# Performance work log

Measured on AMD Instinct MI355X. Metric: run time of the kernel, lower is better.

The kernel has to match this reference:

```python
import jax, jax.numpy as jnp
import numpy as np

NUM_CLUSTERS = 64
MARGIN = 1.0
B = 8192


def setup_inputs() -> dict:
    key = jax.random.key(0)
    k1, k2, k3 = jax.random.split(key, 3)
    features = jax.random.normal(k1, (B, 128), dtype=jnp.float32)
    cluster_labels = jax.random.randint(k2, (B,), 0, NUM_CLUSTERS)
    manifold_coords = jax.random.normal(k3, (B, 2), dtype=jnp.float32)
    return {"features": features, "cluster_labels": cluster_labels,
            "manifold_coords": manifold_coords}


def _pairwise_dist(x):
    # Euclidean cdist via the (|a|^2 + |b|^2 - 2ab) identity; [B, B]
    sq = jnp.sum(x * x, axis=1)
    d2 = sq[:, None] + sq[None, :] - 2.0 * (x @ x.T)
    d2 = jnp.maximum(d2, 0.0)
    # Overwrite diagonal (same-point zero distance) to avoid sqrt(0); diagonal
    # entries only feed the discarded intra-cluster M[i,i] values.
    idx = jnp.arange(x.shape[0])
    d2 = jnp.where(idx[:, None] == idx[None, :], 1.0, d2)
    return jnp.sqrt(d2)


def reference(features, cluster_labels, manifold_coords):
    # Equivalent to the torch double loop over unique labels: min pairwise
    # distance between every cluster pair (i < j), hinge with margin, mean.
    d = _pairwise_dist(manifold_coords)                       # [B, B]
    # segment-min over rows then columns -> min distance per cluster pair
    row_min = jax.ops.segment_min(d, cluster_labels, num_segments=NUM_CLUSTERS)      # [K, B]
    M = jax.ops.segment_min(row_min.T, cluster_labels, num_segments=NUM_CLUSTERS).T  # [K, K]
    upper = jnp.triu(jnp.ones((NUM_CLUSTERS, NUM_CLUSTERS), dtype=bool), k=1)
    hinge = jax.nn.relu(MARGIN - M)
    num_pairs = NUM_CLUSTERS * (NUM_CLUSTERS - 1) // 2
    return jnp.sum(jnp.where(upper, hinge, 0.0)) / num_pairs
```

## Files before the change

### kernel.cpp

```cpp
#include <hip/hip_runtime.h>

#define B_N 8192
#define K_CL 64
#define CAP 256
#define INF_F 3.0e38f


__global__ __launch_bounds__(256) void gather_kernel(
    const int* __restrict__ labels, const float2* __restrict__ coords,
    float2* __restrict__ lists, int* __restrict__ cnts) {
    int c = blockIdx.x;
    __shared__ int cnt;
    int tid = threadIdx.x;
    int lane = tid & 63;
    if (tid == 0) cnt = 0;
    __syncthreads();
#pragma unroll
    for (int k = 0; k < 8; ++k) {
        int v4 = tid + k * 256;
        int4 lb = reinterpret_cast<const int4*>(labels)[v4];
        int lab[4] = {lb.x, lb.y, lb.z, lb.w};
#pragma unroll
        for (int cc = 0; cc < 4; ++cc) {
            bool m = (lab[cc] == c);
            unsigned long long mask = __ballot(m);
            if (mask) {
                int wb = 0;
                if (lane == 0) wb = atomicAdd(&cnt, __popcll(mask));
                wb = __shfl(wb, 0, 64);
                if (m) {
                    int pos = wb + __popcll(mask & ((1ull << lane) - 1));
                    if (pos < CAP) lists[c * CAP + pos] = coords[v4 * 4 + cc];
                }
            }
        }
    }
    __syncthreads();
    if (tid == 0) cnts[c] = min(cnt, CAP);
}

__global__ __launch_bounds__(256) void pair_min_kernel(
    const float2* __restrict__ lists, const int* __restrict__ cnts,
    float* __restrict__ hinges) {
    int ci = blockIdx.x, cj = blockIdx.y;
    if (ci >= cj) return;
    int nI = cnts[ci], nJ = cnts[cj];
    int tid = threadIdx.x;
    __shared__ float2 jpt[CAP];
    if (tid < nJ) jpt[tid] = lists[cj * CAP + tid];
    bool valid = tid < nI;
    float2 pi = make_float2(0.0f, 0.0f);
    if (valid) pi = lists[ci * CAP + tid];
    __syncthreads();

    float m0 = INF_F, m1 = INF_F, m2 = INF_F, m3 = INF_F;
    if (valid) {
        int j = 0;
        for (; j + 3 < nJ; j += 4) {
            float2 a = jpt[j], b = jpt[j + 1], c = jpt[j + 2], d = jpt[j + 3];
            float dx0 = pi.x - a.x, dy0 = pi.y - a.y;
            float dx1 = pi.x - b.x, dy1 = pi.y - b.y;
            float dx2 = pi.x - c.x, dy2 = pi.y - c.y;
            float dx3 = pi.x - d.x, dy3 = pi.y - d.y;
            m0 = fminf(m0, dx0 * dx0 + dy0 * dy0);
            m1 = fminf(m1, dx1 * dx1 + dy1 * dy1);
            m2 = fminf(m2, dx2 * dx2 + dy2 * dy2);
            m3 = fminf(m3, dx3 * dx3 + dy3 * dy3);
        }
        for (; j < nJ; ++j) {
            float dx = pi.x - jpt[j].x, dy = pi.y - jpt[j].y;
            m0 = fminf(m0, dx * dx + dy * dy);
        }
    }
    float myMin = fminf(fminf(m0, m1), fminf(m2, m3));

    for (int off = 32; off > 0; off >>= 1)
        myMin = fminf(myMin, __shfl_down(myMin, off, 64));
    __shared__ float wmin[4];
    int wave = tid >> 6, lane = tid & 63;
    if (lane == 0) wmin[wave] = myMin;
    __syncthreads();
    if (tid == 0) {
        float m = fminf(fminf(wmin[0], wmin[1]), fminf(wmin[2], wmin[3]));
        float h = 1.0f - sqrtf(m);
        hinges[ci * K_CL + cj] = h > 0.0f ? h : 0.0f;
    }
}

__global__ void reduce_hinge_kernel(const float* __restrict__ hinges,
                                    float* __restrict__ out) {
    int tid = threadIdx.x;
    float s = 0.0f;
    for (int p = tid; p < K_CL * K_CL; p += 256) {
        int ci = p >> 6, cj = p & 63;
        if (ci < cj) s += hinges[p];
    }
    for (int off = 32; off > 0; off >>= 1)
        s += __shfl_down(s, off, 64);
    __shared__ float wsum[4];
    int wave = tid >> 6, lane = tid & 63;
    if (lane == 0) wsum[wave] = s;
    __syncthreads();
    if (tid == 0)
        out[0] = (wsum[0] + wsum[1] + wsum[2] + wsum[3]) / 2016.0f;
}

extern "C" void kernel_launch(void* const* d_in, const int* in_sizes, int n_in,
                              void* d_out, int out_size, void* d_ws, size_t ws_size,
                              hipStream_t stream) {
    const int*    labels = (const int*)d_in[1];
    const float2* coords = (const float2*)d_in[2];
    float* out = (float*)d_out;

    float2* lists  = (float2*)d_ws;
    int*    cnts   = (int*)((float*)d_ws + 2 * K_CL * CAP);
    float*  hinges = (float*)d_ws + 2 * K_CL * CAP + 64;

    gather_kernel<<<K_CL, 256, 0, stream>>>(labels, coords, lists, cnts);
    dim3 grid(K_CL, K_CL);
    pair_min_kernel<<<grid, 256, 0, stream>>>(lists, cnts, hinges);
    reduce_hinge_kernel<<<1, 256, 0, stream>>>(hinges, out);
}
```

Measured before the change: 29.70 us.

## Fuse hinge reduction into pair kernel via last-block atomic counter

Launches only the 2016 upper-triangle cluster pairs as a 1D grid instead of a 64x64 grid where half the blocks exit early. The final hinge sum moves into the pair kernel: each block increments an atomic counter, and the last block to finish sums all hinges. This removes one kernel launch and the empty blocks. In exchange it adds a memset launch to reset the counter, a serial loop in each block to decode the pair index, and a tail where one block does the whole sum.

```diff
diff --git a/kernel.cpp b/kernel.cpp
--- a/kernel.cpp
+++ b/kernel.cpp
@@ -3,6 +3,7 @@
 #define B_N 8192
 #define K_CL 64
 #define CAP 256
+#define NPAIR 2016
 #define INF_F 3.0e38f
 
 
@@ -39,14 +40,21 @@
     if (tid == 0) cnts[c] = min(cnt, CAP);
 }
 
-__global__ __launch_bounds__(256) void pair_min_kernel(
+__global__ __launch_bounds__(256) void pair_reduce_kernel(
     const float2* __restrict__ lists, const int* __restrict__ cnts,
-    float* __restrict__ hinges) {
-    int ci = blockIdx.x, cj = blockIdx.y;
-    if (ci >= cj) return;
+    float* __restrict__ hinges, int* __restrict__ done,
+    float* __restrict__ out) {
+    int p = blockIdx.x;
+    int tid = threadIdx.x;
+    int lane = tid & 63, wave = tid >> 6;
+    int ci = 0, rem = p;
+    while (rem >= K_CL - 1 - ci) { rem -= K_CL - 1 - ci; ci++; }
+    int cj = ci + 1 + rem;
     int nI = cnts[ci], nJ = cnts[cj];
-    int tid = threadIdx.x;
+
     __shared__ float2 jpt[CAP];
+    __shared__ float wred[4];
+    __shared__ int lastFlag;
     if (tid < nJ) jpt[tid] = lists[cj * CAP + tid];
     bool valid = tid < nI;
     float2 pi = make_float2(0.0f, 0.0f);
@@ -73,36 +81,33 @@
         }
     }
     float myMin = fminf(fminf(m0, m1), fminf(m2, m3));
-
     for (int off = 32; off > 0; off >>= 1)
         myMin = fminf(myMin, __shfl_down(myMin, off, 64));
-    __shared__ float wmin[4];
-    int wave = tid >> 6, lane = tid & 63;
-    if (lane == 0) wmin[wave] = myMin;
+    if (lane == 0) wred[wave] = myMin;
     __syncthreads();
     if (tid == 0) {
-        float m = fminf(fminf(wmin[0], wmin[1]), fminf(wmin[2], wmin[3]));
+        float m = fminf(fminf(wred[0], wred[1]), fminf(wred[2], wred[3]));
         float h = 1.0f - sqrtf(m);
-        hinges[ci * K_CL + cj] = h > 0.0f ? h : 0.0f;
+        hinges[p] = h > 0.0f ? h : 0.0f;
+        __threadfence();
+        int old = __hip_atomic_fetch_add(done, 1, __ATOMIC_ACQ_REL,
+                                         __HIP_MEMORY_SCOPE_AGENT);
+        lastFlag = (old == NPAIR - 1) ? 1 : 0;
     }
-}
+    __syncthreads();
 
-__global__ void reduce_hinge_kernel(const float* __restrict__ hinges,
-                                    float* __restrict__ out) {
-    int tid = threadIdx.x;
-    float s = 0.0f;
-    for (int p = tid; p < K_CL * K_CL; p += 256) {
-        int ci = p >> 6, cj = p & 63;
-        if (ci < cj) s += hinges[p];
+    if (lastFlag) {
+        float s = 0.0f;
+        for (int q = tid; q < NPAIR; q += 256)
+            s += __hip_atomic_load(&hinges[q], __ATOMIC_RELAXED,
+                                   __HIP_MEMORY_SCOPE_AGENT);
+        for (int off = 32; off > 0; off >>= 1)
+            s += __shfl_down(s, off, 64);
+        if (lane == 0) wred[wave] = s;
+        __syncthreads();
+        if (tid == 0)
+            out[0] = (wred[0] + wred[1] + wred[2] + wred[3]) / (float)NPAIR;
     }
-    for (int off = 32; off > 0; off >>= 1)
-        s += __shfl_down(s, off, 64);
-    __shared__ float wsum[4];
-    int wave = tid >> 6, lane = tid & 63;
-    if (lane == 0) wsum[wave] = s;
-    __syncthreads();
-    if (tid == 0)
-        out[0] = (wsum[0] + wsum[1] + wsum[2] + wsum[3]) / 2016.0f;
 }
 
 extern "C" void kernel_launch(void* const* d_in, const int* in_sizes, int n_in,
@@ -113,11 +118,11 @@
     float* out = (float*)d_out;
 
     float2* lists  = (float2*)d_ws;
-    int*    cnts   = (int*)((float*)d_ws + 2 * K_CL * CAP);
-    float*  hinges = (float*)d_ws + 2 * K_CL * CAP + 64;
+    int*    cnts   = (int*)((char*)d_ws + 2 * K_CL * CAP * sizeof(float));
+    float*  hinges = (float*)((char*)cnts + K_CL * sizeof(int) + 64);
+    int*    done   = (int*)((char*)hinges + NPAIR * sizeof(float));
 
+    hipMemsetAsync(done, 0, sizeof(int), stream);
     gather_kernel<<<K_CL, 256, 0, stream>>>(labels, coords, lists, cnts);
-    dim3 grid(K_CL, K_CL);
-    pair_min_kernel<<<grid, 256, 0, stream>>>(lists, cnts, hinges);
-    reduce_hinge_kernel<<<1, 256, 0, stream>>>(hinges, out);
+    pair_reduce_kernel<<<NPAIR, 256, 0, stream>>>(lists, cnts, hinges, done, out);
 }
```

Measured after the change: 83.99 us. 183% more time.

## Fuse cluster gather into pair-min kernel, rebuilding point lists per block

Applied to the files above, without the earlier changes.

Removes the separate gather kernel and its global list buffers. Each pair block now scans all 8192 labels itself and builds both cluster point lists in shared memory before computing the min distance. This saves one kernel launch and a global round trip, but each of the 2016 active blocks redundantly reads the full label array (32 KB) and does twice the ballot/atomic work, which can cost more than it saves.

```diff
diff --git a/kernel.cpp b/kernel.cpp
--- a/kernel.cpp
+++ b/kernel.cpp
@@ -3,18 +3,22 @@
 #define B_N 8192
 #define K_CL 64
 #define CAP 256
+#define NPAIR 2016
 #define INF_F 3.0e38f
 
 
-__global__ __launch_bounds__(256) void gather_kernel(
+__global__ __launch_bounds__(256) void pair_kernel(
     const int* __restrict__ labels, const float2* __restrict__ coords,
-    float2* __restrict__ lists, int* __restrict__ cnts) {
-    int c = blockIdx.x;
-    __shared__ int cnt;
-    int tid = threadIdx.x;
-    int lane = tid & 63;
-    if (tid == 0) cnt = 0;
+    float* __restrict__ hinges) {
+    int ci = blockIdx.x, cj = blockIdx.y;
+    if (ci >= cj) return;
+    int tid = threadIdx.x, lane = tid & 63, wave = tid >> 6;
+    __shared__ float2 ipts[CAP], jpts[CAP];
+    __shared__ float wred[4];
+    __shared__ int cntI, cntJ;
+    if (tid == 0) { cntI = 0; cntJ = 0; }
     __syncthreads();
+
 #pragma unroll
     for (int k = 0; k < 8; ++k) {
         int v4 = tid + k * 256;
@@ -22,42 +26,42 @@
         int lab[4] = {lb.x, lb.y, lb.z, lb.w};
 #pragma unroll
         for (int cc = 0; cc < 4; ++cc) {
-            bool m = (lab[cc] == c);
-            unsigned long long mask = __ballot(m);
-            if (mask) {
+            bool mi = (lab[cc] == ci);
+            bool mj = (lab[cc] == cj);
+            unsigned long long bi = __ballot(mi);
+            unsigned long long bj = __ballot(mj);
+            if (bi) {
                 int wb = 0;
-                if (lane == 0) wb = atomicAdd(&cnt, __popcll(mask));
+                if (lane == 0) wb = atomicAdd(&cntI, __popcll(bi));
                 wb = __shfl(wb, 0, 64);
-                if (m) {
-                    int pos = wb + __popcll(mask & ((1ull << lane) - 1));
-                    if (pos < CAP) lists[c * CAP + pos] = coords[v4 * 4 + cc];
+                if (mi) {
+                    int pos = wb + __popcll(bi & ((1ull << lane) - 1));
+                    if (pos < CAP) ipts[pos] = coords[v4 * 4 + cc];
+                }
+            }
+            if (bj) {
+                int wb = 0;
+                if (lane == 0) wb = atomicAdd(&cntJ, __popcll(bj));
+                wb = __shfl(wb, 0, 64);
+                if (mj) {
+                    int pos = wb + __popcll(bj & ((1ull << lane) - 1));
+                    if (pos < CAP) jpts[pos] = coords[v4 * 4 + cc];
                 }
             }
         }
     }
     __syncthreads();
-    if (tid == 0) cnts[c] = min(cnt, CAP);
-}
+    int nI = min(cntI, CAP), nJ = min(cntJ, CAP);
 
-__global__ __launch_bounds__(256) void pair_min_kernel(
-    const float2* __restrict__ lists, const int* __restrict__ cnts,
-    float* __restrict__ hinges) {
-    int ci = blockIdx.x, cj = blockIdx.y;
-    if (ci >= cj) return;
-    int nI = cnts[ci], nJ = cnts[cj];
-    int tid = threadIdx.x;
-    __shared__ float2 jpt[CAP];
-    if (tid < nJ) jpt[tid] = lists[cj * CAP + tid];
     bool valid = tid < nI;
     float2 pi = make_float2(0.0f, 0.0f);
-    if (valid) pi = lists[ci * CAP + tid];
-    __syncthreads();
+    if (valid) pi = ipts[tid];
 
     float m0 = INF_F, m1 = INF_F, m2 = INF_F, m3 = INF_F;
     if (valid) {
         int j = 0;
         for (; j + 3 < nJ; j += 4) {
-            float2 a = jpt[j], b = jpt[j + 1], c = jpt[j + 2], d = jpt[j + 3];
+            float2 a = jpts[j], b = jpts[j + 1], c = jpts[j + 2], d = jpts[j + 3];
             float dx0 = pi.x - a.x, dy0 = pi.y - a.y;
             float dx1 = pi.x - b.x, dy1 = pi.y - b.y;
             float dx2 = pi.x - c.x, dy2 = pi.y - c.y;
@@ -68,20 +72,17 @@
             m3 = fminf(m3, dx3 * dx3 + dy3 * dy3);
         }
         for (; j < nJ; ++j) {
-            float dx = pi.x - jpt[j].x, dy = pi.y - jpt[j].y;
+            float dx = pi.x - jpts[j].x, dy = pi.y - jpts[j].y;
             m0 = fminf(m0, dx * dx + dy * dy);
         }
     }
     float myMin = fminf(fminf(m0, m1), fminf(m2, m3));
-
     for (int off = 32; off > 0; off >>= 1)
         myMin = fminf(myMin, __shfl_down(myMin, off, 64));
-    __shared__ float wmin[4];
-    int wave = tid >> 6, lane = tid & 63;
-    if (lane == 0) wmin[wave] = myMin;
+    if (lane == 0) wred[wave] = myMin;
     __syncthreads();
     if (tid == 0) {
-        float m = fminf(fminf(wmin[0], wmin[1]), fminf(wmin[2], wmin[3]));
+        float m = fminf(fminf(wred[0], wred[1]), fminf(wred[2], wred[3]));
         float h = 1.0f - sqrtf(m);
         hinges[ci * K_CL + cj] = h > 0.0f ? h : 0.0f;
     }
@@ -102,7 +103,7 @@
     if (lane == 0) wsum[wave] = s;
     __syncthreads();
     if (tid == 0)
-        out[0] = (wsum[0] + wsum[1] + wsum[2] + wsum[3]) / 2016.0f;
+        out[0] = (wsum[0] + wsum[1] + wsum[2] + wsum[3]) / (float)NPAIR;
 }
 
 extern "C" void kernel_launch(void* const* d_in, const int* in_sizes, int n_in,
@@ -110,14 +111,10 @@
                               hipStream_t stream) {
     const int*    labels = (const int*)d_in[1];
     const float2* coords = (const float2*)d_in[2];
-    float* out = (float*)d_out;
+    float* out    = (float*)d_out;
+    float* hinges = (float*)d_ws;
 
-    float2* lists  = (float2*)d_ws;
-    int*    cnts   = (int*)((float*)d_ws + 2 * K_CL * CAP);
-    float*  hinges = (float*)d_ws + 2 * K_CL * CAP + 64;
-
-    gather_kernel<<<K_CL, 256, 0, stream>>>(labels, coords, lists, cnts);
     dim3 grid(K_CL, K_CL);
-    pair_min_kernel<<<grid, 256, 0, stream>>>(lists, cnts, hinges);
+    pair_kernel<<<grid, 256, 0, stream>>>(labels, coords, hinges);
     reduce_hinge_kernel<<<1, 256, 0, stream>>>(hinges, out);
 }
```

Result: slower. 47.81 us (+61.0%).
